# Kernel tuning notes

Hardware: AMD Instinct MI355X
Metric: run time of the kernel (lower is better)

The kernel has to match this reference:

```python
import jax, jax.numpy as jnp
import numpy as np

N, IN_DIM, OUT_DIM = 8192, 512, 256


def setup_inputs() -> dict:
    key = jax.random.key(0)
    k1, k2, k3 = jax.random.split(key, 3)
    X = jax.random.normal(k1, (N, IN_DIM), dtype=jnp.float32)
    # torch nn.Linear(in_dim, out_dim, bias=False): y = x @ W^T; store as [in_dim, out_dim]
    W = jax.random.normal(k2, (IN_DIM, OUT_DIM), dtype=jnp.float32) / np.sqrt(IN_DIM)
    # a: Linear(2*out_dim, 1, bias=False) -> vector of length 2*out_dim
    a = jax.random.normal(k3, (2 * OUT_DIM,), dtype=jnp.float32) / np.sqrt(2 * OUT_DIM)
    return {"X": X, "W": W, "a": a}


def reference(X, W, a):
    H = X @ W  # [N, D]
    D = H.shape[1]
    # a([Hi ; Hj]) = Hi @ a[:D] + Hj @ a[D:] -> avoid materializing [N,N,2D]
    e = (H @ a[:D])[:, None] + (H @ a[D:])[None, :]  # [N, N]
    e = jnp.where(e > 0, e, 0.2 * e)  # leaky_relu(0.2)
    A = jax.nn.softmax(e, axis=-1)  # row softmax [N, N]
    out = A @ H  # [N, D]
    return out, A
```

## Files before the change

kernel.cpp:

```cpp
#include <hip/hip_runtime.h>
#include <math.h>

#define NN 8192
#define KDIM 512
#define DD 256
#define CS 32
#define NC 256

typedef float4 f4;
typedef __attribute__((ext_vector_type(4))) float f4v;

__device__ __forceinline__ float dot4(const f4& x, const f4& y) {
  return x.x * y.x + x.y * y.y + x.z * y.z + x.w * y.w;
}

__global__ __launch_bounds__(256) void k_gemm(const float* __restrict__ X,
                                              const float* __restrict__ W,
                                              const float* __restrict__ av,
                                              float* __restrict__ H,
                                              float* __restrict__ s,
                                              float* __restrict__ t) {
  __shared__ float Xs[32][64];
  __shared__ float Ws[32][64];
  const int tid = threadIdx.x;
  const int tx = tid & 15;
  const int ty = tid >> 4;
  const int r0 = blockIdx.x * 64;
  const int c0 = blockIdx.y * 64;
  float acc[4][4] = {};
  for (int k0 = 0; k0 < KDIM; k0 += 32) {
#pragma unroll
    for (int q = 0; q < 2; ++q) {
      int fi = tid + q * 256;
      int r = fi >> 3;
      int kq = fi & 7;
      f4 v = *reinterpret_cast<const f4*>(&X[(size_t)(r0 + r) * KDIM + k0 + kq * 4]);
      Xs[kq * 4 + 0][r] = v.x; Xs[kq * 4 + 1][r] = v.y;
      Xs[kq * 4 + 2][r] = v.z; Xs[kq * 4 + 3][r] = v.w;
    }
#pragma unroll
    for (int q = 0; q < 2; ++q) {
      int fi = tid + q * 256;
      int k = fi >> 4;
      int cq = fi & 15;
      f4 v = *reinterpret_cast<const f4*>(&W[(size_t)(k0 + k) * DD + c0 + cq * 4]);
      *reinterpret_cast<f4*>(&Ws[k][cq * 4]) = v;
    }
    __syncthreads();
#pragma unroll
    for (int k = 0; k < 32; ++k) {
      f4 xv = *reinterpret_cast<const f4*>(&Xs[k][ty * 4]);
      f4 wv = *reinterpret_cast<const f4*>(&Ws[k][tx * 4]);
      float xs[4] = {xv.x, xv.y, xv.z, xv.w};
      float ws[4] = {wv.x, wv.y, wv.z, wv.w};
#pragma unroll
      for (int i = 0; i < 4; ++i)
#pragma unroll
        for (int j = 0; j < 4; ++j) acc[i][j] += xs[i] * ws[j];
    }
    __syncthreads();
  }
#pragma unroll
  for (int i = 0; i < 4; ++i) {
    f4 v = {acc[i][0], acc[i][1], acc[i][2], acc[i][3]};
    *reinterpret_cast<f4*>(&H[(size_t)(r0 + ty * 4 + i) * DD + c0 + tx * 4]) = v;
  }

  if (c0 == 0) {
    float* wv1 = &Xs[0][0];
    float* wv2 = &Xs[0][0] + 512;
    for (int k = tid; k < KDIM; k += 256) {
      float acc1 = 0.f, acc2 = 0.f;
#pragma unroll 8
      for (int d4 = 0; d4 < DD / 4; ++d4) {
        f4 wrow = *reinterpret_cast<const f4*>(&W[(size_t)k * DD + d4 * 4]);
        f4 a1v = *reinterpret_cast<const f4*>(&av[d4 * 4]);
        f4 a2v = *reinterpret_cast<const f4*>(&av[DD + d4 * 4]);
        acc1 += dot4(wrow, a1v);
        acc2 += dot4(wrow, a2v);
      }
      wv1[k] = acc1;
      wv2[k] = acc2;
    }
    __syncthreads();
    int wid = tid >> 6, lane = tid & 63;
    f4 w1a = *reinterpret_cast<const f4*>(&wv1[lane * 8]);
    f4 w1b = *reinterpret_cast<const f4*>(&wv1[lane * 8 + 4]);
    f4 w2a = *reinterpret_cast<const f4*>(&wv2[lane * 8]);
    f4 w2b = *reinterpret_cast<const f4*>(&wv2[lane * 8 + 4]);
    for (int rr = 0; rr < 16; ++rr) {
      int i = r0 + wid * 16 + rr;
      f4 xa = *reinterpret_cast<const f4*>(&X[(size_t)i * KDIM + lane * 8]);
      f4 xb = *reinterpret_cast<const f4*>(&X[(size_t)i * KDIM + lane * 8 + 4]);
      float p1 = dot4(xa, w1a) + dot4(xb, w1b);
      float p2 = dot4(xa, w2a) + dot4(xb, w2b);
      for (int off = 32; off > 0; off >>= 1) {
        p1 += __shfl_down(p1, off);
        p2 += __shfl_down(p2, off);
      }
      if (lane == 0) { s[i] = p1; t[i] = p2; }
    }
  }
}

__global__ __launch_bounds__(256) void k_mid(const float* __restrict__ s,
                                             const float* __restrict__ t,
                                             float* __restrict__ E1,
                                             float* __restrict__ E2,
                                             float* __restrict__ c1,
                                             float* __restrict__ c2,
                                             float* __restrict__ tsort,
                                             int* __restrict__ perm) {
  __shared__ float ts[NN];
  __shared__ float lred[4];
  const int b = blockIdx.x;
  const int tid = threadIdx.x;
  const int wid = tid >> 6, lane = tid & 63;

  float m = -1e30f;
#pragma unroll
  for (int q = 0; q < NN / 1024; ++q) {
    int idx = (q * 256 + tid) * 4;
    f4 v = *reinterpret_cast<const f4*>(&t[idx]);
    *reinterpret_cast<f4*>(&ts[idx]) = v;
    m = fmaxf(m, fmaxf(fmaxf(v.x, v.y), fmaxf(v.z, v.w)));
  }
  for (int off = 32; off > 0; off >>= 1) m = fmaxf(m, __shfl_down(m, off));
  if (lane == 0) lred[wid] = m;
  __syncthreads();
  float tmax = fmaxf(fmaxf(lred[0], lred[1]), fmaxf(lred[2], lred[3]));

  if (tid < 32) {
    int i = b * 32 + tid;
    float ti = ts[i];
    E1[i] = expf(ti);
    E2[i] = expf(0.2f * ti);
    float si = s[i];
    float e = si + tmax;
    float mm = e > 0.f ? e : 0.2f * e;
    c1[i] = expf(si - mm);
    c2[i] = expf(0.2f * si - mm);
  }

  float tkv[8]; int jj[8]; int cnt[8];
#pragma unroll
  for (int q = 0; q < 8; ++q) {
    jj[q] = b * 32 + wid * 8 + q;
    tkv[q] = ts[jj[q]];
    cnt[q] = 0;
  }
  for (int m2 = 0; m2 < NN / 64; ++m2) {
    int i = lane + m2 * 64;
    float v = ts[i];
#pragma unroll
    for (int q = 0; q < 8; ++q)
      cnt[q] += (v < tkv[q]) || (v == tkv[q] && i < jj[q]);
  }
#pragma unroll
  for (int q = 0; q < 8; ++q) {
    int c = cnt[q];
    for (int off = 32; off > 0; off >>= 1) c += __shfl_down(c, off);
    if (lane == 0) { tsort[c] = tkv[q]; perm[c] = jj[q]; }
  }
}

__global__ __launch_bounds__(256) void k_chunk(const float* __restrict__ H,
                                               const float* __restrict__ E1,
                                               const float* __restrict__ E2,
                                               const int* __restrict__ perm,
                                               float* __restrict__ Ctot1,
                                               float* __restrict__ Ctot2,
                                               float* __restrict__ cs1,
                                               float* __restrict__ cs2) {
  __shared__ int pms[CS];
  __shared__ float pe1[CS], pe2[CS];
  int c = blockIdx.x;
  int d = threadIdx.x;
  if (d < CS) {
    int p = perm[c * CS + d];
    pms[d] = p;
    pe1[d] = E1[p];
    pe2[d] = E2[p];
  }
  __syncthreads();
  float s1 = 0.f, s2 = 0.f, a1 = 0.f, a2 = 0.f;
#pragma unroll 4
  for (int kk = 0; kk < CS; ++kk) {
    float e1 = pe1[kk], e2 = pe2[kk];
    float h = H[(size_t)pms[kk] * DD + d];
    s1 += e1 * h; s2 += e2 * h;
    a1 += e1;     a2 += e2;
  }
  Ctot1[c * DD + d] = s1;
  Ctot2[c * DD + d] = s2;
  if (d == 0) { cs1[c] = a1; cs2[c] = a2; }
}

__global__ __launch_bounds__(256) void k_prefix(const float* __restrict__ H,
                                                const float* __restrict__ E1,
                                                const float* __restrict__ E2,
                                                const int* __restrict__ perm,
                                                const float* __restrict__ Ctot1,
                                                const float* __restrict__ Ctot2,
                                                const float* __restrict__ cs1,
                                                const float* __restrict__ cs2,
                                                float* __restrict__ PRE1,
                                                float* __restrict__ PRE2,
                                                float* __restrict__ p1s,
                                                float* __restrict__ p2s) {
  __shared__ float sa[NC], sb[NC];
  __shared__ int pms[CS];
  __shared__ float pe1[CS], pe2[CS];
  int c = blockIdx.x;
  int d = threadIdx.x;
  if (d < CS) {
    int p = perm[c * CS + d];
    pms[d] = p;
    pe1[d] = E1[p];
    pe2[d] = E2[p];
  }
  float r1a = 0.f, r1b = 0.f, r2a = 0.f, r2b = 0.f;
  int cc = 0;
  for (; cc + 4 <= c; cc += 4) {
    r1a += Ctot1[(cc + 0) * DD + d];
    r1b += Ctot1[(cc + 1) * DD + d];
    r1a += Ctot1[(cc + 2) * DD + d];
    r1b += Ctot1[(cc + 3) * DD + d];
    r2a += Ctot2[(cc + 0) * DD + d];
    r2b += Ctot2[(cc + 1) * DD + d];
    r2a += Ctot2[(cc + 2) * DD + d];
    r2b += Ctot2[(cc + 3) * DD + d];
  }
  for (; cc < c; ++cc) {
    r1a += Ctot1[cc * DD + d];
    r2a += Ctot2[cc * DD + d];
  }
  float r1 = r1a + r1b, r2 = r2a + r2b;
  sa[d] = (d < c) ? cs1[d] : 0.f;
  sb[d] = (d < c) ? cs2[d] : 0.f;
  __syncthreads();
  for (int off = 128; off > 0; off >>= 1) {
    if (d < off) { sa[d] += sa[d + off]; sb[d] += sb[d + off]; }
    __syncthreads();
  }
  float sr1 = sa[0], sr2 = sb[0];
#pragma unroll 2
  for (int kk = 0; kk < CS; ++kk) {
    int k = c * CS + kk;
    PRE1[(size_t)k * DD + d] = r1;
    PRE2[(size_t)k * DD + d] = r2;
    float e1 = pe1[kk], e2 = pe2[kk];
    float h = H[(size_t)pms[kk] * DD + d];
    r1 += e1 * h; r2 += e2 * h;
    if (d == 0) { p1s[k] = sr1; p2s[k] = sr2; sr1 += e1; sr2 += e2; }
  }
  if (c == NC - 1) {
    PRE1[(size_t)NN * DD + d] = r1;
    PRE2[(size_t)NN * DD + d] = r2;
    if (d == 0) { p1s[NN] = sr1; p2s[NN] = sr2; }
  }
}

__global__ __launch_bounds__(256) void k_finalize(const float* __restrict__ s,
                                                  const float* __restrict__ c1,
                                                  const float* __restrict__ c2,
                                                  const float* __restrict__ tsort,
                                                  const float* __restrict__ p1s,
                                                  const float* __restrict__ p2s,
                                                  const float* __restrict__ PRE1,
                                                  const float* __restrict__ PRE2,
                                                  float* __restrict__ out,
                                                  float* __restrict__ f1,
                                                  float* __restrict__ f2) {
  __shared__ float ts[NN];
  int b = blockIdx.x;
  int tid = threadIdx.x;
  int wid = tid >> 6, lane = tid & 63;
#pragma unroll
  for (int q = 0; q < NN / 1024; ++q) {
    int idx = (q * 256 + tid) * 4;
    *reinterpret_cast<f4*>(&ts[idx]) = *reinterpret_cast<const f4*>(&tsort[idx]);
  }
  __syncthreads();
  int kk[8];
#pragma unroll
  for (int it = 0; it < 8; ++it) {
    int i = b * 32 + it * 4 + wid;
    float key = -s[i];
    int lo = 0, hi = NN;
    while (lo < hi) {
      int mid = (lo + hi) >> 1;
      if (ts[mid] <= key) lo = mid + 1; else hi = mid;
    }
    kk[it] = lo;
  }
  int d = lane * 4;
  f4 T1 = *reinterpret_cast<const f4*>(&PRE1[(size_t)NN * DD + d]);
  float tot1 = p1s[NN];
#pragma unroll
  for (int it = 0; it < 8; ++it) {
    int i = b * 32 + it * 4 + wid;
    int k = kk[it];
    float cc1 = c1[i], cc2 = c2[i];
    float Z = cc1 * (tot1 - p1s[k]) + cc2 * p2s[k];
    float rZ = 1.0f / Z;
    if (lane == 0) { f1[i] = rZ * cc1; f2[i] = rZ * cc2; }
    f4 P1 = *reinterpret_cast<const f4*>(&PRE1[(size_t)k * DD + d]);
    f4 P2 = *reinterpret_cast<const f4*>(&PRE2[(size_t)k * DD + d]);
    f4 o;
    o.x = rZ * (cc1 * (T1.x - P1.x) + cc2 * P2.x);
    o.y = rZ * (cc1 * (T1.y - P1.y) + cc2 * P2.y);
    o.z = rZ * (cc1 * (T1.z - P1.z) + cc2 * P2.z);
    o.w = rZ * (cc1 * (T1.w - P1.w) + cc2 * P2.w);
    *reinterpret_cast<f4*>(&out[(size_t)i * DD + d]) = o;
  }
}

__global__ __launch_bounds__(256) void k_astream(const float* __restrict__ s,
                                                 const float* __restrict__ t,
                                                 const float* __restrict__ E1,
                                                 const float* __restrict__ E2,
                                                 const float* __restrict__ f1,
                                                 const float* __restrict__ f2,
                                                 float* __restrict__ A) {
  int j0 = blockIdx.x * 1024 + threadIdx.x * 4;
  int i0 = blockIdx.y * 32;
  f4 t4  = *reinterpret_cast<const f4*>(&t[j0]);
  f4 e14 = *reinterpret_cast<const f4*>(&E1[j0]);
  f4 e24 = *reinterpret_cast<const f4*>(&E2[j0]);
#pragma unroll 4
  for (int rr = 0; rr < 32; ++rr) {
    int i = i0 + rr;
    float ss = s[i], ff1 = f1[i], ff2 = f2[i];
    f4v o;
    float e;
    e = ss + t4.x; o.x = (e > 0.f) ? ff1 * e14.x : ff2 * e24.x;
    e = ss + t4.y; o.y = (e > 0.f) ? ff1 * e14.y : ff2 * e24.y;
    e = ss + t4.z; o.z = (e > 0.f) ? ff1 * e14.z : ff2 * e24.z;
    e = ss + t4.w; o.w = (e > 0.f) ? ff1 * e14.w : ff2 * e24.w;
    __builtin_nontemporal_store(o, reinterpret_cast<f4v*>(&A[(size_t)i * NN + j0]));
  }
}

extern "C" void kernel_launch(void* const* d_in, const int* in_sizes, int n_in,
                              void* d_out, int out_size, void* d_ws, size_t ws_size,
                              hipStream_t stream) {
  const float* X  = (const float*)d_in[0];
  const float* W  = (const float*)d_in[1];
  const float* av = (const float*)d_in[2];
  float* outp = (float*)d_out;
  float* A = outp + (size_t)NN * DD;

  float* wsp = (float*)d_ws;
  float* s  = wsp + 0 * NN;
  float* t  = wsp + 1 * NN;
  float* E1 = wsp + 2 * NN;
  float* E2 = wsp + 3 * NN;
  float* c1 = wsp + 4 * NN;
  float* c2 = wsp + 5 * NN;
  float* f1 = wsp + 6 * NN;
  float* f2 = wsp + 7 * NN;

  float* H     = outp;
  float* PRE1  = A;
  float* PRE2  = A + 4194304;
  float* Ctot1 = A + 8388608;
  float* Ctot2 = Ctot1 + NC * DD;
  float* cs1   = Ctot2 + NC * DD;
  float* cs2   = cs1 + NC;
  float* p1s   = cs2 + NC;
  float* p2s   = p1s + (NN + 256);
  float* tsort = p2s + (NN + 256);
  int*   perm  = (int*)(tsort + NN);

  k_gemm<<<dim3(NN / 64, DD / 64), 256, 0, stream>>>(X, W, av, H, s, t);
  k_mid<<<NC, 256, 0, stream>>>(s, t, E1, E2, c1, c2, tsort, perm);
  k_chunk<<<NC, 256, 0, stream>>>(H, E1, E2, perm, Ctot1, Ctot2, cs1, cs2);
  k_prefix<<<NC, 256, 0, stream>>>(H, E1, E2, perm, Ctot1, Ctot2, cs1, cs2,
                                   PRE1, PRE2, p1s, p2s);
  k_finalize<<<NN / 32, 256, 0, stream>>>(s, c1, c2, tsort, p1s, p2s, PRE1, PRE2,
                                          outp, f1, f2);
  k_astream<<<dim3(NN / 1024, NN / 32), 256, 0, stream>>>(s, t, E1, E2, f1, f2, A);
}
```

Measured before the change: 196.5 us.

## Fuse all stages into one cooperative persistent kernel with grid barriers

Replaces the six separate kernel launches with a single cooperative kernel of 256 blocks that runs GEMM, sort/rank, chunk sums, prefix, finalize and A streaming in sequence, separated by a custom atomic grid barrier. The GEMM tile is widened to 64x128 so that 256 blocks cover H. The aim is to remove launch gaps and inter-kernel drain. In exchange only 256 blocks run, which may underuse the GPU in the GEMM and the A-store phase. It also adds barrier spin cost and a memset to reset the barrier counters.

```diff
diff --git a/kernel.cpp b/kernel.cpp
--- a/kernel.cpp
+++ b/kernel.cpp
@@ -6,6 +6,7 @@
 #define DD 256
 #define CS 32
 #define NC 256
+#define NB 256
 
 typedef float4 f4;
 typedef __attribute__((ext_vector_type(4))) float f4v;
@@ -14,344 +15,30 @@
   return x.x * y.x + x.y * y.y + x.z * y.z + x.w * y.w;
 }
 
-__global__ __launch_bounds__(256) void k_gemm(const float* __restrict__ X,
-                                              const float* __restrict__ W,
-                                              const float* __restrict__ av,
-                                              float* __restrict__ H,
-                                              float* __restrict__ s,
-                                              float* __restrict__ t) {
-  __shared__ float Xs[32][64];
-  __shared__ float Ws[32][64];
-  const int tid = threadIdx.x;
-  const int tx = tid & 15;
-  const int ty = tid >> 4;
-  const int r0 = blockIdx.x * 64;
-  const int c0 = blockIdx.y * 64;
-  float acc[4][4] = {};
-  for (int k0 = 0; k0 < KDIM; k0 += 32) {
-#pragma unroll
-    for (int q = 0; q < 2; ++q) {
-      int fi = tid + q * 256;
-      int r = fi >> 3;
-      int kq = fi & 7;
-      f4 v = *reinterpret_cast<const f4*>(&X[(size_t)(r0 + r) * KDIM + k0 + kq * 4]);
-      Xs[kq * 4 + 0][r] = v.x; Xs[kq * 4 + 1][r] = v.y;
-      Xs[kq * 4 + 2][r] = v.z; Xs[kq * 4 + 3][r] = v.w;
-    }
-#pragma unroll
-    for (int q = 0; q < 2; ++q) {
-      int fi = tid + q * 256;
-      int k = fi >> 4;
-      int cq = fi & 15;
-      f4 v = *reinterpret_cast<const f4*>(&W[(size_t)(k0 + k) * DD + c0 + cq * 4]);
-      *reinterpret_cast<f4*>(&Ws[k][cq * 4]) = v;
-    }
-    __syncthreads();
-#pragma unroll
-    for (int k = 0; k < 32; ++k) {
-      f4 xv = *reinterpret_cast<const f4*>(&Xs[k][ty * 4]);
-      f4 wv = *reinterpret_cast<const f4*>(&Ws[k][tx * 4]);
-      float xs[4] = {xv.x, xv.y, xv.z, xv.w};
-      float ws[4] = {wv.x, wv.y, wv.z, wv.w};
-#pragma unroll
-      for (int i = 0; i < 4; ++i)
-#pragma unroll
-        for (int j = 0; j < 4; ++j) acc[i][j] += xs[i] * ws[j];
-    }
-    __syncthreads();
-  }
-#pragma unroll
-  for (int i = 0; i < 4; ++i) {
-    f4 v = {acc[i][0], acc[i][1], acc[i][2], acc[i][3]};
-    *reinterpret_cast<f4*>(&H[(size_t)(r0 + ty * 4 + i) * DD + c0 + tx * 4]) = v;
-  }
-
-  if (c0 == 0) {
-    float* wv1 = &Xs[0][0];
-    float* wv2 = &Xs[0][0] + 512;
-    for (int k = tid; k < KDIM; k += 256) {
-      float acc1 = 0.f, acc2 = 0.f;
-#pragma unroll 8
-      for (int d4 = 0; d4 < DD / 4; ++d4) {
-        f4 wrow = *reinterpret_cast<const f4*>(&W[(size_t)k * DD + d4 * 4]);
-        f4 a1v = *reinterpret_cast<const f4*>(&av[d4 * 4]);
-        f4 a2v = *reinterpret_cast<const f4*>(&av[DD + d4 * 4]);
-        acc1 += dot4(wrow, a1v);
-        acc2 += dot4(wrow, a2v);
-      }
-      wv1[k] = acc1;
-      wv2[k] = acc2;
-    }
-    __syncthreads();
-    int wid = tid >> 6, lane = tid & 63;
-    f4 w1a = *reinterpret_cast<const f4*>(&wv1[lane * 8]);
-    f4 w1b = *reinterpret_cast<const f4*>(&wv1[lane * 8 + 4]);
-    f4 w2a = *reinterpret_cast<const f4*>(&wv2[lane * 8]);
-    f4 w2b = *reinterpret_cast<const f4*>(&wv2[lane * 8 + 4]);
-    for (int rr = 0; rr < 16; ++rr) {
-      int i = r0 + wid * 16 + rr;
-      f4 xa = *reinterpret_cast<const f4*>(&X[(size_t)i * KDIM + lane * 8]);
-      f4 xb = *reinterpret_cast<const f4*>(&X[(size_t)i * KDIM + lane * 8 + 4]);
-      float p1 = dot4(xa, w1a) + dot4(xb, w1b);
-      float p2 = dot4(xa, w2a) + dot4(xb, w2b);
-      for (int off = 32; off > 0; off >>= 1) {
-        p1 += __shfl_down(p1, off);
-        p2 += __shfl_down(p2, off);
-      }
-      if (lane == 0) { s[i] = p1; t[i] = p2; }
-    }
-  }
+__device__ __forceinline__ void gridbar(unsigned* cnt, unsigned* gen) {
+  __syncthreads();
+  if (threadIdx.x == 0) {
+    __threadfence();
+    unsigned g = __hip_atomic_load(gen, __ATOMIC_RELAXED, __HIP_MEMORY_SCOPE_AGENT);
+    unsigned a = __hip_atomic_fetch_add(cnt, 1u, __ATOMIC_ACQ_REL, __HIP_MEMORY_SCOPE_AGENT);
+    if (a == NB - 1) {
+      __hip_atomic_store(cnt, 0u, __ATOMIC_RELAXED, __HIP_MEMORY_SCOPE_AGENT);
+      __hip_atomic_store(gen, g + 1u, __ATOMIC_RELEASE, __HIP_MEMORY_SCOPE_AGENT);
+    } else {
+      while (__hip_atomic_load(gen, __ATOMIC_ACQUIRE, __HIP_MEMORY_SCOPE_AGENT) == g)
+        __builtin_amdgcn_s_sleep(1);
+    }
+    __threadfence();
+  }
+  __syncthreads();
 }
 
-__global__ __launch_bounds__(256) void k_mid(const float* __restrict__ s,
-                                             const float* __restrict__ t,
-                                             float* __restrict__ E1,
-                                             float* __restrict__ E2,
-                                             float* __restrict__ c1,
-                                             float* __restrict__ c2,
-                                             float* __restrict__ tsort,
-                                             int* __restrict__ perm) {
-  __shared__ float ts[NN];
-  __shared__ float lred[4];
-  const int b = blockIdx.x;
-  const int tid = threadIdx.x;
-  const int wid = tid >> 6, lane = tid & 63;
-
-  float m = -1e30f;
-#pragma unroll
-  for (int q = 0; q < NN / 1024; ++q) {
-    int idx = (q * 256 + tid) * 4;
-    f4 v = *reinterpret_cast<const f4*>(&t[idx]);
-    *reinterpret_cast<f4*>(&ts[idx]) = v;
-    m = fmaxf(m, fmaxf(fmaxf(v.x, v.y), fmaxf(v.z, v.w)));
-  }
-  for (int off = 32; off > 0; off >>= 1) m = fmaxf(m, __shfl_down(m, off));
-  if (lane == 0) lred[wid] = m;
-  __syncthreads();
-  float tmax = fmaxf(fmaxf(lred[0], lred[1]), fmaxf(lred[2], lred[3]));
-
-  if (tid < 32) {
-    int i = b * 32 + tid;
-    float ti = ts[i];
-    E1[i] = expf(ti);
-    E2[i] = expf(0.2f * ti);
-    float si = s[i];
-    float e = si + tmax;
-    float mm = e > 0.f ? e : 0.2f * e;
-    c1[i] = expf(si - mm);
-    c2[i] = expf(0.2f * si - mm);
-  }
-
-  float tkv[8]; int jj[8]; int cnt[8];
-#pragma unroll
-  for (int q = 0; q < 8; ++q) {
-    jj[q] = b * 32 + wid * 8 + q;
-    tkv[q] = ts[jj[q]];
-    cnt[q] = 0;
-  }
-  for (int m2 = 0; m2 < NN / 64; ++m2) {
-    int i = lane + m2 * 64;
-    float v = ts[i];
-#pragma unroll
-    for (int q = 0; q < 8; ++q)
-      cnt[q] += (v < tkv[q]) || (v == tkv[q] && i < jj[q]);
-  }
-#pragma unroll
-  for (int q = 0; q < 8; ++q) {
-    int c = cnt[q];
-    for (int off = 32; off > 0; off >>= 1) c += __shfl_down(c, off);
-    if (lane == 0) { tsort[c] = tkv[q]; perm[c] = jj[q]; }
-  }
-}
-
-__global__ __launch_bounds__(256) void k_chunk(const float* __restrict__ H,
-                                               const float* __restrict__ E1,
-                                               const float* __restrict__ E2,
-                                               const int* __restrict__ perm,
-                                               float* __restrict__ Ctot1,
-                                               float* __restrict__ Ctot2,
-                                               float* __restrict__ cs1,
-                                               float* __restrict__ cs2) {
-  __shared__ int pms[CS];
-  __shared__ float pe1[CS], pe2[CS];
-  int c = blockIdx.x;
-  int d = threadIdx.x;
-  if (d < CS) {
-    int p = perm[c * CS + d];
-    pms[d] = p;
-    pe1[d] = E1[p];
-    pe2[d] = E2[p];
-  }
-  __syncthreads();
-  float s1 = 0.f, s2 = 0.f, a1 = 0.f, a2 = 0.f;
-#pragma unroll 4
-  for (int kk = 0; kk < CS; ++kk) {
-    float e1 = pe1[kk], e2 = pe2[kk];
-    float h = H[(size_t)pms[kk] * DD + d];
-    s1 += e1 * h; s2 += e2 * h;
-    a1 += e1;     a2 += e2;
-  }
-  Ctot1[c * DD + d] = s1;
-  Ctot2[c * DD + d] = s2;
-  if (d == 0) { cs1[c] = a1; cs2[c] = a2; }
-}
-
-__global__ __launch_bounds__(256) void k_prefix(const float* __restrict__ H,
-                                                const float* __restrict__ E1,
-                                                const float* __restrict__ E2,
-                                                const int* __restrict__ perm,
-                                                const float* __restrict__ Ctot1,
-                                                const float* __restrict__ Ctot2,
-                                                const float* __restrict__ cs1,
-                                                const float* __restrict__ cs2,
-                                                float* __restrict__ PRE1,
-                                                float* __restrict__ PRE2,
-                                                float* __restrict__ p1s,
-                                                float* __restrict__ p2s) {
-  __shared__ float sa[NC], sb[NC];
-  __shared__ int pms[CS];
-  __shared__ float pe1[CS], pe2[CS];
-  int c = blockIdx.x;
-  int d = threadIdx.x;
-  if (d < CS) {
-    int p = perm[c * CS + d];
-    pms[d] = p;
-    pe1[d] = E1[p];
-    pe2[d] = E2[p];
-  }
-  float r1a = 0.f, r1b = 0.f, r2a = 0.f, r2b = 0.f;
-  int cc = 0;
-  for (; cc + 4 <= c; cc += 4) {
-    r1a += Ctot1[(cc + 0) * DD + d];
-    r1b += Ctot1[(cc + 1) * DD + d];
-    r1a += Ctot1[(cc + 2) * DD + d];
-    r1b += Ctot1[(cc + 3) * DD + d];
-    r2a += Ctot2[(cc + 0) * DD + d];
-    r2b += Ctot2[(cc + 1) * DD + d];
-    r2a += Ctot2[(cc + 2) * DD + d];
-    r2b += Ctot2[(cc + 3) * DD + d];
-  }
-  for (; cc < c; ++cc) {
-    r1a += Ctot1[cc * DD + d];
-    r2a += Ctot2[cc * DD + d];
-  }
-  float r1 = r1a + r1b, r2 = r2a + r2b;
-  sa[d] = (d < c) ? cs1[d] : 0.f;
-  sb[d] = (d < c) ? cs2[d] : 0.f;
-  __syncthreads();
-  for (int off = 128; off > 0; off >>= 1) {
-    if (d < off) { sa[d] += sa[d + off]; sb[d] += sb[d + off]; }
-    __syncthreads();
-  }
-  float sr1 = sa[0], sr2 = sb[0];
-#pragma unroll 2
-  for (int kk = 0; kk < CS; ++kk) {
-    int k = c * CS + kk;
-    PRE1[(size_t)k * DD + d] = r1;
-    PRE2[(size_t)k * DD + d] = r2;
-    float e1 = pe1[kk], e2 = pe2[kk];
-    float h = H[(size_t)pms[kk] * DD + d];
-    r1 += e1 * h; r2 += e2 * h;
-    if (d == 0) { p1s[k] = sr1; p2s[k] = sr2; sr1 += e1; sr2 += e2; }
-  }
-  if (c == NC - 1) {
-    PRE1[(size_t)NN * DD + d] = r1;
-    PRE2[(size_t)NN * DD + d] = r2;
-    if (d == 0) { p1s[NN] = sr1; p2s[NN] = sr2; }
-  }
-}
-
-__global__ __launch_bounds__(256) void k_finalize(const float* __restrict__ s,
-                                                  const float* __restrict__ c1,
-                                                  const float* __restrict__ c2,
-                                                  const float* __restrict__ tsort,
-                                                  const float* __restrict__ p1s,
-                                                  const float* __restrict__ p2s,
-                                                  const float* __restrict__ PRE1,
-                                                  const float* __restrict__ PRE2,
-                                                  float* __restrict__ out,
-                                                  float* __restrict__ f1,
-                                                  float* __restrict__ f2) {
-  __shared__ float ts[NN];
-  int b = blockIdx.x;
-  int tid = threadIdx.x;
-  int wid = tid >> 6, lane = tid & 63;
-#pragma unroll
-  for (int q = 0; q < NN / 1024; ++q) {
-    int idx = (q * 256 + tid) * 4;
-    *reinterpret_cast<f4*>(&ts[idx]) = *reinterpret_cast<const f4*>(&tsort[idx]);
-  }
-  __syncthreads();
-  int kk[8];
-#pragma unroll
-  for (int it = 0; it < 8; ++it) {
-    int i = b * 32 + it * 4 + wid;
-    float key = -s[i];
-    int lo = 0, hi = NN;
-    while (lo < hi) {
-      int mid = (lo + hi) >> 1;
-      if (ts[mid] <= key) lo = mid + 1; else hi = mid;
-    }
-    kk[it] = lo;
-  }
-  int d = lane * 4;
-  f4 T1 = *reinterpret_cast<const f4*>(&PRE1[(size_t)NN * DD + d]);
-  float tot1 = p1s[NN];
-#pragma unroll
-  for (int it = 0; it < 8; ++it) {
-    int i = b * 32 + it * 4 + wid;
-    int k = kk[it];
-    float cc1 = c1[i], cc2 = c2[i];
-    float Z = cc1 * (tot1 - p1s[k]) + cc2 * p2s[k];
-    float rZ = 1.0f / Z;
-    if (lane == 0) { f1[i] = rZ * cc1; f2[i] = rZ * cc2; }
-    f4 P1 = *reinterpret_cast<const f4*>(&PRE1[(size_t)k * DD + d]);
-    f4 P2 = *reinterpret_cast<const f4*>(&PRE2[(size_t)k * DD + d]);
-    f4 o;
-    o.x = rZ * (cc1 * (T1.x - P1.x) + cc2 * P2.x);
-    o.y = rZ * (cc1 * (T1.y - P1.y) + cc2 * P2.y);
-    o.z = rZ * (cc1 * (T1.z - P1.z) + cc2 * P2.z);
-    o.w = rZ * (cc1 * (T1.w - P1.w) + cc2 * P2.w);
-    *reinterpret_cast<f4*>(&out[(size_t)i * DD + d]) = o;
-  }
-}
-
-__global__ __launch_bounds__(256) void k_astream(const float* __restrict__ s,
-                                                 const float* __restrict__ t,
-                                                 const float* __restrict__ E1,
-                                                 const float* __restrict__ E2,
-                                                 const float* __restrict__ f1,
-                                                 const float* __restrict__ f2,
-                                                 float* __restrict__ A) {
-  int j0 = blockIdx.x * 1024 + threadIdx.x * 4;
-  int i0 = blockIdx.y * 32;
-  f4 t4  = *reinterpret_cast<const f4*>(&t[j0]);
-  f4 e14 = *reinterpret_cast<const f4*>(&E1[j0]);
-  f4 e24 = *reinterpret_cast<const f4*>(&E2[j0]);
-#pragma unroll 4
-  for (int rr = 0; rr < 32; ++rr) {
-    int i = i0 + rr;
-    float ss = s[i], ff1 = f1[i], ff2 = f2[i];
-    f4v o;
-    float e;
-    e = ss + t4.x; o.x = (e > 0.f) ? ff1 * e14.x : ff2 * e24.x;
-    e = ss + t4.y; o.y = (e > 0.f) ? ff1 * e14.y : ff2 * e24.y;
-    e = ss + t4.z; o.z = (e > 0.f) ? ff1 * e14.z : ff2 * e24.z;
-    e = ss + t4.w; o.w = (e > 0.f) ? ff1 * e14.w : ff2 * e24.w;
-    __builtin_nontemporal_store(o, reinterpret_cast<f4v*>(&A[(size_t)i * NN + j0]));
-  }
-}
-
-extern "C" void kernel_launch(void* const* d_in, const int* in_sizes, int n_in,
-                              void* d_out, int out_size, void* d_ws, size_t ws_size,
-                              hipStream_t stream) {
-  const float* X  = (const float*)d_in[0];
-  const float* W  = (const float*)d_in[1];
-  const float* av = (const float*)d_in[2];
-  float* outp = (float*)d_out;
-  float* A = outp + (size_t)NN * DD;
-
-  float* wsp = (float*)d_ws;
+__global__ __launch_bounds__(256) void k_fused(const float* __restrict__ X,
+                                               const float* __restrict__ W,
+                                               const float* __restrict__ av,
+                                               float* __restrict__ out,
+                                               float* __restrict__ Ab,
+                                               float* __restrict__ wsp) {
   float* s  = wsp + 0 * NN;
   float* t  = wsp + 1 * NN;
   float* E1 = wsp + 2 * NN;
@@ -360,11 +47,10 @@
   float* c2 = wsp + 5 * NN;
   float* f1 = wsp + 6 * NN;
   float* f2 = wsp + 7 * NN;
-
-  float* H     = outp;
-  float* PRE1  = A;
-  float* PRE2  = A + 4194304;
-  float* Ctot1 = A + 8388608;
+  float* H     = out;
+  float* PRE1  = Ab;
+  float* PRE2  = Ab + 4194304;
+  float* Ctot1 = Ab + 8388608;
   float* Ctot2 = Ctot1 + NC * DD;
   float* cs1   = Ctot2 + NC * DD;
   float* cs2   = cs1 + NC;
@@ -372,13 +58,323 @@
   float* p2s   = p1s + (NN + 256);
   float* tsort = p2s + (NN + 256);
   int*   perm  = (int*)(tsort + NN);
-
-  k_gemm<<<dim3(NN / 64, DD / 64), 256, 0, stream>>>(X, W, av, H, s, t);
-  k_mid<<<NC, 256, 0, stream>>>(s, t, E1, E2, c1, c2, tsort, perm);
-  k_chunk<<<NC, 256, 0, stream>>>(H, E1, E2, perm, Ctot1, Ctot2, cs1, cs2);
-  k_prefix<<<NC, 256, 0, stream>>>(H, E1, E2, perm, Ctot1, Ctot2, cs1, cs2,
-                                   PRE1, PRE2, p1s, p2s);
-  k_finalize<<<NN / 32, 256, 0, stream>>>(s, c1, c2, tsort, p1s, p2s, PRE1, PRE2,
-                                          outp, f1, f2);
-  k_astream<<<dim3(NN / 1024, NN / 32), 256, 0, stream>>>(s, t, E1, E2, f1, f2, A);
+  unsigned* bcnt = (unsigned*)(Ab + 8600000);
+  unsigned* bgen = bcnt + 1;
+
+  __shared__ float smem[8192];
+  __shared__ float sa[NC], sb[NC];
+  __shared__ int   pms[CS];
+  __shared__ float pe1[CS], pe2[CS];
+  __shared__ float lred[4];
+  __shared__ float srow[32], f1r[32], f2r[32];
+
+  const int b = blockIdx.x;
+  const int tid = threadIdx.x;
+  const int wid = tid >> 6, lane = tid & 63;
+
+  {
+    float (*Xs)[64]  = (float(*)[64])smem;
+    float (*Ws)[128] = (float(*)[128])(smem + 2048);
+    const int tx = tid & 15;
+    const int ty = tid >> 4;
+    const int rt = b >> 1;
+    const int cp = b & 1;
+    const int r0 = rt * 64;
+    const int c0 = cp * 128;
+    float acc0[4][4] = {};
+    float acc1[4][4] = {};
+    for (int k0 = 0; k0 < KDIM; k0 += 32) {
+#pragma unroll
+      for (int q = 0; q < 2; ++q) {
+        int fi = tid + q * 256;
+        int r = fi >> 3;
+        int kq = fi & 7;
+        f4 v = *reinterpret_cast<const f4*>(&X[(size_t)(r0 + r) * KDIM + k0 + kq * 4]);
+        Xs[kq * 4 + 0][r] = v.x; Xs[kq * 4 + 1][r] = v.y;
+        Xs[kq * 4 + 2][r] = v.z; Xs[kq * 4 + 3][r] = v.w;
+      }
+#pragma unroll
+      for (int q = 0; q < 4; ++q) {
+        int fi = tid + q * 256;
+        int k = fi >> 5;
+        int cw = fi & 31;
+        f4 v = *reinterpret_cast<const f4*>(&W[(size_t)(k0 + k) * DD + c0 + cw * 4]);
+        *reinterpret_cast<f4*>(&Ws[k][cw * 4]) = v;
+      }
+      __syncthreads();
+#pragma unroll
+      for (int k = 0; k < 32; ++k) {
+        f4 xv = *reinterpret_cast<const f4*>(&Xs[k][ty * 4]);
+        f4 wa = *reinterpret_cast<const f4*>(&Ws[k][tx * 4]);
+        f4 wb = *reinterpret_cast<const f4*>(&Ws[k][64 + tx * 4]);
+        float xs[4] = {xv.x, xv.y, xv.z, xv.w};
+        float wsa[4] = {wa.x, wa.y, wa.z, wa.w};
+        float wsb[4] = {wb.x, wb.y, wb.z, wb.w};
+#pragma unroll
+        for (int i = 0; i < 4; ++i)
+#pragma unroll
+          for (int j = 0; j < 4; ++j) {
+            acc0[i][j] += xs[i] * wsa[j];
+            acc1[i][j] += xs[i] * wsb[j];
+          }
+      }
+      __syncthreads();
+    }
+#pragma unroll
+    for (int i = 0; i < 4; ++i) {
+      f4 v0 = {acc0[i][0], acc0[i][1], acc0[i][2], acc0[i][3]};
+      f4 v1 = {acc1[i][0], acc1[i][1], acc1[i][2], acc1[i][3]};
+      *reinterpret_cast<f4*>(&H[(size_t)(r0 + ty * 4 + i) * DD + c0 + tx * 4]) = v0;
+      *reinterpret_cast<f4*>(&H[(size_t)(r0 + ty * 4 + i) * DD + c0 + 64 + tx * 4]) = v1;
+    }
+
+    if (cp == 0) {
+      float* wv1 = smem;
+      float* wv2 = smem + 512;
+      for (int k = tid; k < KDIM; k += 256) {
+        float a1acc = 0.f, a2acc = 0.f;
+#pragma unroll 8
+        for (int d4 = 0; d4 < DD / 4; ++d4) {
+          f4 wrow = *reinterpret_cast<const f4*>(&W[(size_t)k * DD + d4 * 4]);
+          f4 a1v = *reinterpret_cast<const f4*>(&av[d4 * 4]);
+          f4 a2v = *reinterpret_cast<const f4*>(&av[DD + d4 * 4]);
+          a1acc += dot4(wrow, a1v);
+          a2acc += dot4(wrow, a2v);
+        }
+        wv1[k] = a1acc;
+        wv2[k] = a2acc;
+      }
+      __syncthreads();
+      f4 w1a = *reinterpret_cast<const f4*>(&wv1[lane * 8]);
+      f4 w1b = *reinterpret_cast<const f4*>(&wv1[lane * 8 + 4]);
+      f4 w2a = *reinterpret_cast<const f4*>(&wv2[lane * 8]);
+      f4 w2b = *reinterpret_cast<const f4*>(&wv2[lane * 8 + 4]);
+      for (int rr = 0; rr < 16; ++rr) {
+        int i = r0 + wid * 16 + rr;
+        f4 xa = *reinterpret_cast<const f4*>(&X[(size_t)i * KDIM + lane * 8]);
+        f4 xb = *reinterpret_cast<const f4*>(&X[(size_t)i * KDIM + lane * 8 + 4]);
+        float p1 = dot4(xa, w1a) + dot4(xb, w1b);
+        float p2 = dot4(xa, w2a) + dot4(xb, w2b);
+        for (int off = 32; off > 0; off >>= 1) {
+          p1 += __shfl_down(p1, off);
+          p2 += __shfl_down(p2, off);
+        }
+        if (lane == 0) { s[i] = p1; t[i] = p2; }
+      }
+    }
+  }
+  gridbar(bcnt, bgen);
+
+  {
+    float* ts = smem;
+    float m = -1e30f;
+#pragma unroll
+    for (int q = 0; q < NN / 1024; ++q) {
+      int idx = (q * 256 + tid) * 4;
+      f4 v = *reinterpret_cast<const f4*>(&t[idx]);
+      *reinterpret_cast<f4*>(&ts[idx]) = v;
+      m = fmaxf(m, fmaxf(fmaxf(v.x, v.y), fmaxf(v.z, v.w)));
+    }
+    for (int off = 32; off > 0; off >>= 1) m = fmaxf(m, __shfl_down(m, off));
+    if (lane == 0) lred[wid] = m;
+    __syncthreads();
+    float tmax = fmaxf(fmaxf(lred[0], lred[1]), fmaxf(lred[2], lred[3]));
+
+    if (tid < 32) {
+      int i = b * 32 + tid;
+      float ti = ts[i];
+      E1[i] = expf(ti);
+      E2[i] = expf(0.2f * ti);
+      float si = s[i];
+      float e = si + tmax;
+      float mm = e > 0.f ? e : 0.2f * e;
+      c1[i] = expf(si - mm);
+      c2[i] = expf(0.2f * si - mm);
+    }
+
+    float tkv[8]; int jj[8]; int cnt[8];
+#pragma unroll
+    for (int q = 0; q < 8; ++q) {
+      jj[q] = b * 32 + wid * 8 + q;
+      tkv[q] = ts[jj[q]];
+      cnt[q] = 0;
+    }
+    for (int m2 = 0; m2 < NN / 64; ++m2) {
+      int i = lane + m2 * 64;
+      float v = ts[i];
+#pragma unroll
+      for (int q = 0; q < 8; ++q)
+        cnt[q] += (v < tkv[q]) || (v == tkv[q] && i < jj[q]);
+    }
+#pragma unroll
+    for (int q = 0; q < 8; ++q) {
+      int c = cnt[q];
+      for (int off = 32; off > 0; off >>= 1) c += __shfl_down(c, off);
+      if (lane == 0) { tsort[c] = tkv[q]; perm[c] = jj[q]; }
+    }
+  }
+  gridbar(bcnt, bgen);
+
+  {
+    int d = tid;
+    if (d < CS) {
+      int p = perm[b * CS + d];
+      pms[d] = p;
+      pe1[d] = E1[p];
+      pe2[d] = E2[p];
+    }
+    __syncthreads();
+    float s1 = 0.f, s2 = 0.f, a1 = 0.f, a2 = 0.f;
+#pragma unroll 4
+    for (int kk = 0; kk < CS; ++kk) {
+      float e1 = pe1[kk], e2 = pe2[kk];
+      float h = H[(size_t)pms[kk] * DD + d];
+      s1 += e1 * h; s2 += e2 * h;
+      a1 += e1;     a2 += e2;
+    }
+    Ctot1[b * DD + d] = s1;
+    Ctot2[b * DD + d] = s2;
+    if (d == 0) { cs1[b] = a1; cs2[b] = a2; }
+  }
+  gridbar(bcnt, bgen);
+
+  {
+    int d = tid;
+    float r1a = 0.f, r1b = 0.f, r2a = 0.f, r2b = 0.f;
+    int cc = 0;
+    for (; cc + 4 <= b; cc += 4) {
+      r1a += Ctot1[(cc + 0) * DD + d];
+      r1b += Ctot1[(cc + 1) * DD + d];
+      r1a += Ctot1[(cc + 2) * DD + d];
+      r1b += Ctot1[(cc + 3) * DD + d];
+      r2a += Ctot2[(cc + 0) * DD + d];
+      r2b += Ctot2[(cc + 1) * DD + d];
+      r2a += Ctot2[(cc + 2) * DD + d];
+      r2b += Ctot2[(cc + 3) * DD + d];
+    }
+    for (; cc < b; ++cc) {
+      r1a += Ctot1[cc * DD + d];
+      r2a += Ctot2[cc * DD + d];
+    }
+    float r1 = r1a + r1b, r2 = r2a + r2b;
+    if (d < CS) {
+      int p = perm[b * CS + d];
+      pms[d] = p;
+      pe1[d] = E1[p];
+      pe2[d] = E2[p];
+    }
+    sa[d] = (d < b) ? cs1[d] : 0.f;
+    sb[d] = (d < b) ? cs2[d] : 0.f;
+    __syncthreads();
+    for (int off = 128; off > 0; off >>= 1) {
+      if (d < off) { sa[d] += sa[d + off]; sb[d] += sb[d + off]; }
+      __syncthreads();
+    }
+    float sr1 = sa[0], sr2 = sb[0];
+#pragma unroll 2
+    for (int kk = 0; kk < CS; ++kk) {
+      int k = b * CS + kk;
+      PRE1[(size_t)k * DD + d] = r1;
+      PRE2[(size_t)k * DD + d] = r2;
+      float e1 = pe1[kk], e2 = pe2[kk];
+      float h = H[(size_t)pms[kk] * DD + d];
+      r1 += e1 * h; r2 += e2 * h;
+      if (d == 0) { p1s[k] = sr1; p2s[k] = sr2; sr1 += e1; sr2 += e2; }
+    }
+    if (b == NC - 1) {
+      PRE1[(size_t)NN * DD + d] = r1;
+      PRE2[(size_t)NN * DD + d] = r2;
+      if (d == 0) { p1s[NN] = sr1; p2s[NN] = sr2; }
+    }
+  }
+  gridbar(bcnt, bgen);
+
+  {
+    float* ts = smem;
+#pragma unroll
+    for (int q = 0; q < NN / 1024; ++q) {
+      int idx = (q * 256 + tid) * 4;
+      *reinterpret_cast<f4*>(&ts[idx]) = *reinterpret_cast<const f4*>(&tsort[idx]);
+    }
+    __syncthreads();
+    int kk[8];
+#pragma unroll
+    for (int it = 0; it < 8; ++it) {
+      int i = b * 32 + it * 4 + wid;
+      float key = -s[i];
+      int lo = 0, hi = NN;
+      while (lo < hi) {
+        int mid = (lo + hi) >> 1;
+        if (ts[mid] <= key) lo = mid + 1; else hi = mid;
+      }
+      kk[it] = lo;
+    }
+    int d = lane * 4;
+    f4 T1 = *reinterpret_cast<const f4*>(&PRE1[(size_t)NN * DD + d]);
+    float tot1 = p1s[NN];
+#pragma unroll
+    for (int it = 0; it < 8; ++it) {
+      int i = b * 32 + it * 4 + wid;
+      int k = kk[it];
+      float cc1 = c1[i], cc2 = c2[i];
+      float Z = cc1 * (tot1 - p1s[k]) + cc2 * p2s[k];
+      float rZ = 1.0f / Z;
+      if (lane == 0) { f1[i] = rZ * cc1; f2[i] = rZ * cc2; }
+      f4 P1 = *reinterpret_cast<const f4*>(&PRE1[(size_t)k * DD + d]);
+      f4 P2 = *reinterpret_cast<const f4*>(&PRE2[(size_t)k * DD + d]);
+      f4 o;
+      o.x = rZ * (cc1 * (T1.x - P1.x) + cc2 * P2.x);
+      o.y = rZ * (cc1 * (T1.y - P1.y) + cc2 * P2.y);
+      o.z = rZ * (cc1 * (T1.z - P1.z) + cc2 * P2.z);
+      o.w = rZ * (cc1 * (T1.w - P1.w) + cc2 * P2.w);
+      *reinterpret_cast<f4*>(&out[(size_t)i * DD + d]) = o;
+    }
+  }
+  gridbar(bcnt, bgen);
+
+  {
+    if (tid < 32) {
+      int i = b * 32 + tid;
+      srow[tid] = s[i];
+      f1r[tid] = f1[i];
+      f2r[tid] = f2[i];
+    }
+    __syncthreads();
+#pragma unroll
+    for (int jq = 0; jq < 8; ++jq) {
+      int j0 = jq * 1024 + tid * 4;
+      f4 t4  = *reinterpret_cast<const f4*>(&t[j0]);
+      f4 e14 = *reinterpret_cast<const f4*>(&E1[j0]);
+      f4 e24 = *reinterpret_cast<const f4*>(&E2[j0]);
+#pragma unroll 4
+      for (int rr = 0; rr < 32; ++rr) {
+        int i = b * 32 + rr;
+        float ss = srow[rr], ff1 = f1r[rr], ff2 = f2r[rr];
+        f4v o;
+        float e;
+        e = ss + t4.x; o.x = (e > 0.f) ? ff1 * e14.x : ff2 * e24.x;
+        e = ss + t4.y; o.y = (e > 0.f) ? ff1 * e14.y : ff2 * e24.y;
+        e = ss + t4.z; o.z = (e > 0.f) ? ff1 * e14.z : ff2 * e24.z;
+        e = ss + t4.w; o.w = (e > 0.f) ? ff1 * e14.w : ff2 * e24.w;
+        __builtin_nontemporal_store(o, reinterpret_cast<f4v*>(&Ab[(size_t)i * NN + j0]));
+      }
+    }
+  }
 }
+
+extern "C" void kernel_launch(void* const* d_in, const int* in_sizes, int n_in,
+                              void* d_out, int out_size, void* d_ws, size_t ws_size,
+                              hipStream_t stream) {
+  const float* X  = (const float*)d_in[0];
+  const float* W  = (const float*)d_in[1];
+  const float* av = (const float*)d_in[2];
+  float* outp = (float*)d_out;
+  float* Ap   = outp + (size_t)NN * DD;
+  float* wsp  = (float*)d_ws;
+
+  hipMemsetAsync((void*)(Ap + 8600000), 0, 8, stream);
+
+  void* cargs[] = {(void*)&X, (void*)&W, (void*)&av,
+                   (void*)&outp, (void*)&Ap, (void*)&wsp};
+  hipLaunchCooperativeKernel((void*)k_fused, dim3(NB), dim3(256), cargs, 0, stream);
+}
```

After: 421.6 us. 115% more time.

## Fuse prefix and finalize, drop materialized prefix tables, retile rank kernel

Applied to the files above, without the earlier changes.

The separate prefix kernel, which wrote full per-position prefix tables PRE1/PRE2 (two N×D arrays), is removed and merged into the finalize kernel. Each row block now rebuilds its needed prefix sums by walking the chunk totals and adding the partial chunk from H via perm. This avoids writing and re-reading large intermediate arrays. The cost is redundant chunk-total scans in every block and serial per-thread loops over cs1. The rank kernel also stops staging t in 32KB shared memory, reads it from global with float4 loads, and uses twice as many smaller blocks for occupancy.

```diff
diff --git a/kernel.cpp b/kernel.cpp
--- a/kernel.cpp
+++ b/kernel.cpp
@@ -43,8 +43,8 @@
       int fi = tid + q * 256;
       int k = fi >> 4;
       int cq = fi & 15;
-      f4 v = *reinterpret_cast<const f4*>(&W[(size_t)(k0 + k) * DD + c0 + cq * 4]);
-      *reinterpret_cast<f4*>(&Ws[k][cq * 4]) = v;
+      *reinterpret_cast<f4*>(&Ws[k][cq * 4]) =
+          *reinterpret_cast<const f4*>(&W[(size_t)(k0 + k) * DD + c0 + cq * 4]);
     }
     __syncthreads();
 #pragma unroll
@@ -67,23 +67,23 @@
   }
 
   if (c0 == 0) {
+    int wid = tid >> 6, lane = tid & 63;
     float* wv1 = &Xs[0][0];
     float* wv2 = &Xs[0][0] + 512;
     for (int k = tid; k < KDIM; k += 256) {
-      float acc1 = 0.f, acc2 = 0.f;
+      float a1acc = 0.f, a2acc = 0.f;
 #pragma unroll 8
       for (int d4 = 0; d4 < DD / 4; ++d4) {
         f4 wrow = *reinterpret_cast<const f4*>(&W[(size_t)k * DD + d4 * 4]);
         f4 a1v = *reinterpret_cast<const f4*>(&av[d4 * 4]);
         f4 a2v = *reinterpret_cast<const f4*>(&av[DD + d4 * 4]);
-        acc1 += dot4(wrow, a1v);
-        acc2 += dot4(wrow, a2v);
+        a1acc += dot4(wrow, a1v);
+        a2acc += dot4(wrow, a2v);
       }
-      wv1[k] = acc1;
-      wv2[k] = acc2;
+      wv1[k] = a1acc;
+      wv2[k] = a2acc;
     }
     __syncthreads();
-    int wid = tid >> 6, lane = tid & 63;
     f4 w1a = *reinterpret_cast<const f4*>(&wv1[lane * 8]);
     f4 w1b = *reinterpret_cast<const f4*>(&wv1[lane * 8 + 4]);
     f4 w2a = *reinterpret_cast<const f4*>(&wv2[lane * 8]);
@@ -111,18 +111,14 @@
                                              float* __restrict__ c2,
                                              float* __restrict__ tsort,
                                              int* __restrict__ perm) {
-  __shared__ float ts[NN];
   __shared__ float lred[4];
-  const int b = blockIdx.x;
-  const int tid = threadIdx.x;
+  const int b = blockIdx.x, tid = threadIdx.x;
   const int wid = tid >> 6, lane = tid & 63;
-
   float m = -1e30f;
 #pragma unroll
-  for (int q = 0; q < NN / 1024; ++q) {
+  for (int q = 0; q < 8; ++q) {
     int idx = (q * 256 + tid) * 4;
     f4 v = *reinterpret_cast<const f4*>(&t[idx]);
-    *reinterpret_cast<f4*>(&ts[idx]) = v;
     m = fmaxf(m, fmaxf(fmaxf(v.x, v.y), fmaxf(v.z, v.w)));
   }
   for (int off = 32; off > 0; off >>= 1) m = fmaxf(m, __shfl_down(m, off));
@@ -130,9 +126,9 @@
   __syncthreads();
   float tmax = fmaxf(fmaxf(lred[0], lred[1]), fmaxf(lred[2], lred[3]));
 
-  if (tid < 32) {
-    int i = b * 32 + tid;
-    float ti = ts[i];
+  if (tid < 16) {
+    int i = b * 16 + tid;
+    float ti = t[i];
     E1[i] = expf(ti);
     E2[i] = expf(0.2f * ti);
     float si = s[i];
@@ -142,22 +138,27 @@
     c2[i] = expf(0.2f * si - mm);
   }
 
-  float tkv[8]; int jj[8]; int cnt[8];
-#pragma unroll
-  for (int q = 0; q < 8; ++q) {
-    jj[q] = b * 32 + wid * 8 + q;
-    tkv[q] = ts[jj[q]];
+  float tkv[4]; int jj[4]; int cnt[4];
+#pragma unroll
+  for (int q = 0; q < 4; ++q) {
+    jj[q] = b * 16 + wid * 4 + q;
+    tkv[q] = t[jj[q]];
     cnt[q] = 0;
   }
-  for (int m2 = 0; m2 < NN / 64; ++m2) {
-    int i = lane + m2 * 64;
-    float v = ts[i];
-#pragma unroll
-    for (int q = 0; q < 8; ++q)
-      cnt[q] += (v < tkv[q]) || (v == tkv[q] && i < jj[q]);
-  }
-#pragma unroll
-  for (int q = 0; q < 8; ++q) {
+  for (int m2 = 0; m2 < 32; ++m2) {
+    int i4 = m2 * 64 + lane;
+    f4 v = *reinterpret_cast<const f4*>(&t[i4 * 4]);
+    int base = i4 * 4;
+#pragma unroll
+    for (int q = 0; q < 4; ++q) {
+      cnt[q] += (v.x < tkv[q]) || (v.x == tkv[q] && base + 0 < jj[q]);
+      cnt[q] += (v.y < tkv[q]) || (v.y == tkv[q] && base + 1 < jj[q]);
+      cnt[q] += (v.z < tkv[q]) || (v.z == tkv[q] && base + 2 < jj[q]);
+      cnt[q] += (v.w < tkv[q]) || (v.w == tkv[q] && base + 3 < jj[q]);
+    }
+  }
+#pragma unroll
+  for (int q = 0; q < 4; ++q) {
     int c = cnt[q];
     for (int off = 32; off > 0; off >>= 1) c += __shfl_down(c, off);
     if (lane == 0) { tsort[c] = tkv[q]; perm[c] = jj[q]; }
@@ -196,123 +197,101 @@
   if (d == 0) { cs1[c] = a1; cs2[c] = a2; }
 }
 
-__global__ __launch_bounds__(256) void k_prefix(const float* __restrict__ H,
-                                                const float* __restrict__ E1,
-                                                const float* __restrict__ E2,
-                                                const int* __restrict__ perm,
-                                                const float* __restrict__ Ctot1,
-                                                const float* __restrict__ Ctot2,
-                                                const float* __restrict__ cs1,
-                                                const float* __restrict__ cs2,
-                                                float* __restrict__ PRE1,
-                                                float* __restrict__ PRE2,
-                                                float* __restrict__ p1s,
-                                                float* __restrict__ p2s) {
-  __shared__ float sa[NC], sb[NC];
-  __shared__ int pms[CS];
-  __shared__ float pe1[CS], pe2[CS];
-  int c = blockIdx.x;
-  int d = threadIdx.x;
-  if (d < CS) {
-    int p = perm[c * CS + d];
-    pms[d] = p;
-    pe1[d] = E1[p];
-    pe2[d] = E2[p];
-  }
-  float r1a = 0.f, r1b = 0.f, r2a = 0.f, r2b = 0.f;
-  int cc = 0;
-  for (; cc + 4 <= c; cc += 4) {
-    r1a += Ctot1[(cc + 0) * DD + d];
-    r1b += Ctot1[(cc + 1) * DD + d];
-    r1a += Ctot1[(cc + 2) * DD + d];
-    r1b += Ctot1[(cc + 3) * DD + d];
-    r2a += Ctot2[(cc + 0) * DD + d];
-    r2b += Ctot2[(cc + 1) * DD + d];
-    r2a += Ctot2[(cc + 2) * DD + d];
-    r2b += Ctot2[(cc + 3) * DD + d];
-  }
-  for (; cc < c; ++cc) {
-    r1a += Ctot1[cc * DD + d];
-    r2a += Ctot2[cc * DD + d];
-  }
-  float r1 = r1a + r1b, r2 = r2a + r2b;
-  sa[d] = (d < c) ? cs1[d] : 0.f;
-  sb[d] = (d < c) ? cs2[d] : 0.f;
-  __syncthreads();
-  for (int off = 128; off > 0; off >>= 1) {
-    if (d < off) { sa[d] += sa[d + off]; sb[d] += sb[d + off]; }
-    __syncthreads();
-  }
-  float sr1 = sa[0], sr2 = sb[0];
-#pragma unroll 2
-  for (int kk = 0; kk < CS; ++kk) {
-    int k = c * CS + kk;
-    PRE1[(size_t)k * DD + d] = r1;
-    PRE2[(size_t)k * DD + d] = r2;
-    float e1 = pe1[kk], e2 = pe2[kk];
-    float h = H[(size_t)pms[kk] * DD + d];
-    r1 += e1 * h; r2 += e2 * h;
-    if (d == 0) { p1s[k] = sr1; p2s[k] = sr2; sr1 += e1; sr2 += e2; }
-  }
-  if (c == NC - 1) {
-    PRE1[(size_t)NN * DD + d] = r1;
-    PRE2[(size_t)NN * DD + d] = r2;
-    if (d == 0) { p1s[NN] = sr1; p2s[NN] = sr2; }
-  }
-}
-
-__global__ __launch_bounds__(256) void k_finalize(const float* __restrict__ s,
-                                                  const float* __restrict__ c1,
-                                                  const float* __restrict__ c2,
-                                                  const float* __restrict__ tsort,
-                                                  const float* __restrict__ p1s,
-                                                  const float* __restrict__ p2s,
-                                                  const float* __restrict__ PRE1,
-                                                  const float* __restrict__ PRE2,
-                                                  float* __restrict__ out,
-                                                  float* __restrict__ f1,
-                                                  float* __restrict__ f2) {
-  __shared__ float ts[NN];
-  int b = blockIdx.x;
-  int tid = threadIdx.x;
-  int wid = tid >> 6, lane = tid & 63;
-#pragma unroll
-  for (int q = 0; q < NN / 1024; ++q) {
-    int idx = (q * 256 + tid) * 4;
-    *reinterpret_cast<f4*>(&ts[idx]) = *reinterpret_cast<const f4*>(&tsort[idx]);
-  }
-  __syncthreads();
-  int kk[8];
-#pragma unroll
-  for (int it = 0; it < 8; ++it) {
-    int i = b * 32 + it * 4 + wid;
+__global__ __launch_bounds__(256) void k_fin(const float* __restrict__ s,
+                                             const float* __restrict__ c1,
+                                             const float* __restrict__ c2,
+                                             const float* __restrict__ tsort,
+                                             const int* __restrict__ perm,
+                                             const float* __restrict__ E1,
+                                             const float* __restrict__ E2,
+                                             const float* __restrict__ H,
+                                             const float* __restrict__ Ctot1,
+                                             const float* __restrict__ Ctot2,
+                                             const float* __restrict__ cs1,
+                                             const float* __restrict__ cs2,
+                                             float* __restrict__ out,
+                                             float* __restrict__ f1,
+                                             float* __restrict__ f2) {
+  __shared__ int   kiL[32], ciL[32], sIdx[32];
+  __shared__ float g1L[32], g2L[32];
+  __shared__ int   bndL[33];
+  const int b = blockIdx.x;
+  const int tid = threadIdx.x;
+
+  if (tid < 32) {
+    int i = b * 32 + tid;
     float key = -s[i];
     int lo = 0, hi = NN;
     while (lo < hi) {
       int mid = (lo + hi) >> 1;
-      if (ts[mid] <= key) lo = mid + 1; else hi = mid;
-    }
-    kk[it] = lo;
-  }
-  int d = lane * 4;
-  f4 T1 = *reinterpret_cast<const f4*>(&PRE1[(size_t)NN * DD + d]);
-  float tot1 = p1s[NN];
-#pragma unroll
-  for (int it = 0; it < 8; ++it) {
-    int i = b * 32 + it * 4 + wid;
-    int k = kk[it];
-    float cc1 = c1[i], cc2 = c2[i];
-    float Z = cc1 * (tot1 - p1s[k]) + cc2 * p2s[k];
+      if (tsort[mid] <= key) lo = mid + 1; else hi = mid;
+    }
+    int ki = lo, ci = ki >> 5;
+    float tt1 = 0.f, sp1 = 0.f, sp2 = 0.f;
+    for (int cc = 0; cc < NC; ++cc) {
+      float v1 = cs1[cc];
+      tt1 += v1;
+      if (cc < ci) { sp1 += v1; sp2 += cs2[cc]; }
+    }
+    for (int m = ci * CS; m < ki; ++m) {
+      int p = perm[m];
+      sp1 += E1[p];
+      sp2 += E2[p];
+    }
+    float a1 = c1[i], a2 = c2[i];
+    float Z = a1 * (tt1 - sp1) + a2 * sp2;
     float rZ = 1.0f / Z;
-    if (lane == 0) { f1[i] = rZ * cc1; f2[i] = rZ * cc2; }
-    f4 P1 = *reinterpret_cast<const f4*>(&PRE1[(size_t)k * DD + d]);
-    f4 P2 = *reinterpret_cast<const f4*>(&PRE2[(size_t)k * DD + d]);
-    f4 o;
-    o.x = rZ * (cc1 * (T1.x - P1.x) + cc2 * P2.x);
-    o.y = rZ * (cc1 * (T1.y - P1.y) + cc2 * P2.y);
-    o.z = rZ * (cc1 * (T1.z - P1.z) + cc2 * P2.z);
-    o.w = rZ * (cc1 * (T1.w - P1.w) + cc2 * P2.w);
-    *reinterpret_cast<f4*>(&out[(size_t)i * DD + d]) = o;
+    f1[i] = rZ * a1;
+    f2[i] = rZ * a2;
+    g1L[tid] = rZ * a1;
+    g2L[tid] = rZ * a2;
+    kiL[tid] = ki;
+    ciL[tid] = ci;
+  }
+  __syncthreads();
+  if (tid < 32) {
+    int ci = ciL[tid];
+    int rank = 0;
+    for (int r2 = 0; r2 < 32; ++r2) {
+      int cv = ciL[r2];
+      rank += (cv < ci) || (cv == ci && r2 < tid);
+    }
+    sIdx[rank] = tid;
+  }
+  __syncthreads();
+  if (tid < 33) bndL[tid] = (tid < 32) ? ciL[sIdx[tid]] : (NC + 1);
+  __syncthreads();
+
+  const int d = tid;
+  float run1 = 0.f, run2 = 0.f;
+  int ptr = 0;
+  int nextci = bndL[0];
+  for (int cc = 0; cc <= NC; ++cc) {
+    while (nextci == cc) {
+      int r = sIdx[ptr];
+      int ki = kiL[r];
+      float P1 = run1, P2 = run2;
+      for (int m = cc * CS; m < ki; ++m) {
+        int p = perm[m];
+        float h = H[(size_t)p * DD + d];
+        P1 += E1[p] * h;
+        P2 += E2[p] * h;
+      }
+      int i = b * 32 + r;
+      out[(size_t)i * DD + d] = g2L[r] * P2 - g1L[r] * P1;
+      ++ptr;
+      nextci = bndL[ptr];
+    }
+    if (cc < NC) {
+      run1 += Ctot1[cc * DD + d];
+      run2 += Ctot2[cc * DD + d];
+    }
+  }
+  float T1 = run1;
+#pragma unroll 4
+  for (int r = 0; r < 32; ++r) {
+    int i = b * 32 + r;
+    out[(size_t)i * DD + d] += g1L[r] * T1;
   }
 }
 
@@ -361,24 +340,18 @@
   float* f1 = wsp + 6 * NN;
   float* f2 = wsp + 7 * NN;
 
-  float* H     = outp;
-  float* PRE1  = A;
-  float* PRE2  = A + 4194304;
-  float* Ctot1 = A + 8388608;
+  float* Ctot1 = A;
   float* Ctot2 = Ctot1 + NC * DD;
   float* cs1   = Ctot2 + NC * DD;
   float* cs2   = cs1 + NC;
-  float* p1s   = cs2 + NC;
-  float* p2s   = p1s + (NN + 256);
-  float* tsort = p2s + (NN + 256);
+  float* tsort = cs2 + NC;
   int*   perm  = (int*)(tsort + NN);
+  float* H     = A + 16777216;
 
   k_gemm<<<dim3(NN / 64, DD / 64), 256, 0, stream>>>(X, W, av, H, s, t);
-  k_mid<<<NC, 256, 0, stream>>>(s, t, E1, E2, c1, c2, tsort, perm);
+  k_mid<<<NN / 16, 256, 0, stream>>>(s, t, E1, E2, c1, c2, tsort, perm);
   k_chunk<<<NC, 256, 0, stream>>>(H, E1, E2, perm, Ctot1, Ctot2, cs1, cs2);
-  k_prefix<<<NC, 256, 0, stream>>>(H, E1, E2, perm, Ctot1, Ctot2, cs1, cs2,
-                                   PRE1, PRE2, p1s, p2s);
-  k_finalize<<<NN / 32, 256, 0, stream>>>(s, c1, c2, tsort, p1s, p2s, PRE1, PRE2,
-                                          outp, f1, f2);
+  k_fin<<<NN / 32, 256, 0, stream>>>(s, c1, c2, tsort, perm, E1, E2, H,
+                                     Ctot1, Ctot2, cs1, cs2, outp, f1, f2);
   k_astream<<<dim3(NN / 1024, NN / 32), 256, 0, stream>>>(s, t, E1, E2, f1, f2, A);
 }
```

New measurement: 316.1 us. 60.9% more time.
